# Performance work log

Hardware: AMD Instinct MI355X
Metric: run time of the kernel (lower is better)

The kernel has to match this reference:

```python
import jax, jax.numpy as jnp
import numpy as np
import math

NUM_HEADS = 16
D_MODEL = 1024
BATCH = 1
SEQ_LEN = 4096


def alibi_slopes(num_heads):
    # slopes m_h = (256 ** (1/H)) ** -(h+1)
    x = (2.0 ** 8) ** (1.0 / num_heads)
    return jnp.asarray([1.0 / x ** (i + 1) for i in range(num_heads)], dtype=jnp.float32)


def setup_inputs() -> dict:
    key = jax.random.key(0)
    k1, k2 = jax.random.split(key)
    x = jax.random.normal(k1, (BATCH, SEQ_LEN, D_MODEL), dtype=jnp.float32)
    # nn.Linear(d_model, 3*d_model, bias=False); store as [d_model, 3*d_model] so y = x @ w
    w_kqv = jax.random.normal(k2, (D_MODEL, 3 * D_MODEL), dtype=jnp.float32) * (1.0 / math.sqrt(D_MODEL))
    return {"x": x, "w_kqv": w_kqv}


def reference(x, w_kqv):
    B, S, D = x.shape
    H = NUM_HEADS
    dh = D // H
    scale = jnp.asarray(math.sqrt(D), dtype=x.dtype)  # module divides by sqrt(d_model)

    kqv = x @ w_kqv  # [B, S, 3D]
    # NOTE: original chunks as (key, query, value) in that order
    k, q, v = jnp.split(kqv, 3, axis=-1)
    q = q.reshape(B, S, H, dh)
    k = k.reshape(B, S, H, dh)
    v = v.reshape(B, S, H, dh)

    # ALiBi bias: m_h * (j - i), shape [H, S, S]
    pos = jnp.arange(S)
    rel = pos[None, :] - pos[:, None]  # [S, S], x - y
    slopes = alibi_slopes(H).astype(x.dtype)  # [H]
    bias = slopes[:, None, None] * rel.astype(x.dtype)  # [H, S, S]

    score = jnp.einsum('bihd,bjhd->bhij', q, k) / scale + bias[None]  # [B, H, S, S]
    causal = rel <= 0  # j <= i (lower triangular)
    score = jnp.where(causal[None, None], score, jnp.asarray(-jnp.inf, dtype=score.dtype))

    attn = jax.nn.softmax(score, axis=-1)
    out = jnp.einsum('bhij,bjhd->bihd', attn, v).reshape(B, S, D)
    return out
```

## Files before the change

kernel.cpp:

```cpp
#include <hip/hip_runtime.h>
#include <stdint.h>
#include <math.h>

#define SEQ 4096
#define DM  1024
#define NH  16
#define DH  64
#define LOG2E 1.44269504088896341f

typedef short bf16x8 __attribute__((ext_vector_type(8)));
typedef short bf16x4 __attribute__((ext_vector_type(4)));
typedef float f32x4  __attribute__((ext_vector_type(4)));
typedef uint32_t u32x4 __attribute__((ext_vector_type(4)));

typedef const __attribute__((address_space(1))) short* gptr_t;
typedef __attribute__((address_space(3))) short* lptr_t;

__device__ __forceinline__ short f2bf(float f) {
    union { float f; uint32_t u; } x; x.f = f;
    uint32_t r = (x.u + 0x7fffu + ((x.u >> 16) & 1u)) >> 16;
    return (short)r;
}
__device__ __forceinline__ uint32_t pkbf(float lo, float hi) {
    union { float f; uint32_t u; } a, b; a.f = lo; b.f = hi;
    return __builtin_amdgcn_perm(b.u, a.u, 0x07060302u);
}

__device__ __forceinline__ void load_lds16(const short* g, const short* l) {
    __builtin_amdgcn_global_load_lds((gptr_t)(uintptr_t)g,
                                     (lptr_t)(uint32_t)(uintptr_t)l, 16, 0, 0);
}

__device__ __forceinline__ void wgbar() {
    asm volatile("" ::: "memory");
    __builtin_amdgcn_s_barrier();
    asm volatile("" ::: "memory");
}
#define WAITVM(n) asm volatile("s_waitcnt vmcnt(" #n ")" ::: "memory")
#define WAITLGKM(n) do { asm volatile("s_waitcnt lgkmcnt(" #n ")" ::: "memory"); \
                         __builtin_amdgcn_sched_barrier(0); } while (0)
#define DSR(d, a, o) asm volatile("ds_read_b128 %0, %1 offset:" o : "=v"(d) : "v"(a))

__global__ __launch_bounds__(256) void cvt_fused(const float* __restrict__ x,
                                                 const float* __restrict__ w,
                                                 short* __restrict__ xb,
                                                 short* __restrict__ wtb) {
    __shared__ float T[64][69];
    const int b = blockIdx.x;
    if (b < 2048) {
        const int i = (b * 256 + threadIdx.x) * 8;
        float4 a0 = ((const float4*)(x + i))[0];
        float4 a1 = ((const float4*)(x + i))[1];
        bf16x8 p;
        p[0]=f2bf(a0.x); p[1]=f2bf(a0.y); p[2]=f2bf(a0.z); p[3]=f2bf(a0.w);
        p[4]=f2bf(a1.x); p[5]=f2bf(a1.y); p[6]=f2bf(a1.z); p[7]=f2bf(a1.w);
        *(bf16x8*)(xb + i) = p;
        return;
    }
    const int bb = b - 2048;
    const int n0 = (bb % 48) * 64, k0 = (bb / 48) * 64;
    const int t = threadIdx.x;
    {
        const int kr = t >> 4, nc = (t & 15) * 4;
        #pragma unroll
        for (int i = 0; i < 4; ++i) {
            float4 v = *(const float4*)(w + (size_t)(k0 + kr + i * 16) * 3072 + n0 + nc);
            T[kr + i * 16][nc + 0] = v.x; T[kr + i * 16][nc + 1] = v.y;
            T[kr + i * 16][nc + 2] = v.z; T[kr + i * 16][nc + 3] = v.w;
        }
    }
    __syncthreads();
    const int nr = t >> 4, kc = (t & 15) * 4;
    #pragma unroll
    for (int i = 0; i < 4; ++i) {
        const int n = n0 + nr + i * 16;
        const float sc = (n >= 1024 && n < 2048) ? (LOG2E / 32.0f) : 1.0f;
        short4 o;
        o.x = f2bf(T[kc + 0][nr + i * 16] * sc);
        o.y = f2bf(T[kc + 1][nr + i * 16] * sc);
        o.z = f2bf(T[kc + 2][nr + i * 16] * sc);
        o.w = f2bf(T[kc + 3][nr + i * 16] * sc);
        *(short4*)(wtb + (size_t)n * 1024 + k0 + kc) = o;
    }
}

__global__ __launch_bounds__(256, 2) void qkv_gemm(const short* __restrict__ xb,
                                                   const short* __restrict__ wtb,
                                                   short* __restrict__ kq,
                                                   short* __restrict__ vt) {
    __shared__ short As[2][8192];
    __shared__ short Bs[2][8192];
    const int col0 = blockIdx.y * 128, row0 = blockIdx.x * 128;
    const int tid = threadIdx.x, w = tid >> 6, lane = tid & 63;
    const int lmod = lane & 15, ldiv = lane >> 4;
    const int wr = (w >> 1) * 64, wc = (w & 1) * 64;

    const int srow = w * 32 + (lane >> 3);
    const int slc  = (lane & 7) ^ ((lane >> 3) & 7);
    const short* gA = xb  + (size_t)(row0 + srow) * 1024 + slc * 8;
    const short* gB = wtb + (size_t)(col0 + srow) * 1024 + slc * 8;
    short* lA = &As[0][0] + w * 2048;
    short* lB = &Bs[0][0] + w * 2048;

    const uint32_t asb = (uint32_t)(uintptr_t)&As[0][0];
    const uint32_t bsb = (uint32_t)(uintptr_t)&Bs[0][0];
    const int xorm = lmod & 7;
    const int rdA = (wr + lmod) * 128 + ((ldiv ^ xorm) << 4);
    const int rdB = (wc + lmod) * 128 + ((ldiv ^ xorm) << 4);

    f32x4 acc[4][4] = {};

    auto stage = [&](int kt, int p) {
        const short* ga = gA + kt * 64;
        const short* gb = gB + kt * 64;
        short* la = lA + p * 8192;
        short* lb = lB + p * 8192;
        #pragma unroll
        for (int q = 0; q < 4; ++q) {
            load_lds16(ga + q * 8192, la + q * 512);
            load_lds16(gb + q * 8192, lb + q * 512);
        }
    };

    stage(0, 0);
    stage(1, 1);
    WAITVM(8);
    wgbar();

    for (int t = 0; t < 16; ++t) {
        const int poff = (t & 1) << 14;
        const int aA0 = (int)asb + poff + rdA, aA1 = aA0 ^ 64;
        const int bA0 = (int)bsb + poff + rdB, bA1 = bA0 ^ 64;
        bf16x8 a0[4], a1[4], b0[4], b1[4];
        DSR(a0[0], aA0, "0");    DSR(a0[1], aA0, "2048");
        DSR(a0[2], aA0, "4096"); DSR(a0[3], aA0, "6144");
        DSR(b0[0], bA0, "0");    DSR(b0[1], bA0, "2048");
        DSR(b0[2], bA0, "4096"); DSR(b0[3], bA0, "6144");
        DSR(a1[0], aA1, "0");    DSR(a1[1], aA1, "2048");
        DSR(a1[2], aA1, "4096"); DSR(a1[3], aA1, "6144");
        DSR(b1[0], bA1, "0");    DSR(b1[1], bA1, "2048");
        DSR(b1[2], bA1, "4096"); DSR(b1[3], bA1, "6144");
        WAITLGKM(8);
        #pragma unroll
        for (int i = 0; i < 4; ++i)
            #pragma unroll
            for (int j = 0; j < 4; ++j)
                acc[i][j] = __builtin_amdgcn_mfma_f32_16x16x32_bf16(a0[i], b0[j], acc[i][j], 0, 0, 0);
        WAITLGKM(0);
        #pragma unroll
        for (int i = 0; i < 4; ++i)
            #pragma unroll
            for (int j = 0; j < 4; ++j)
                acc[i][j] = __builtin_amdgcn_mfma_f32_16x16x32_bf16(a1[i], b1[j], acc[i][j], 0, 0, 0);

        wgbar();
        if (t + 2 < 16) {
            stage(t + 2, t & 1);
            WAITVM(8);
            wgbar();
        } else if (t + 1 < 16) {
            WAITVM(0);
            wgbar();
        }
    }

    if (col0 < 2048) {
        #pragma unroll
        for (int i = 0; i < 4; ++i)
            #pragma unroll
            for (int j = 0; j < 4; ++j)
                #pragma unroll
                for (int r = 0; r < 4; ++r)
                    kq[(size_t)(row0 + wr + i * 16 + ldiv * 4 + r) * 2048
                       + col0 + wc + j * 16 + lmod] = f2bf(acc[i][j][r]);
    } else {
        #pragma unroll
        for (int i = 0; i < 4; ++i) {
            const int ig = row0 + wr + i * 16 + ldiv * 4;
            const int kk = ig & 63;
            const int kkp = (kk & 32) | ((kk & 12) << 1) | ((kk & 16) >> 2);
            const int igp = (ig & ~63) | kkp;
            #pragma unroll
            for (int j = 0; j < 4; ++j) {
                const int cg = col0 + wc + j * 16 + lmod - 2048;
                const int h = cg >> 6, d = cg & 63;
                bf16x4 p;
                p[0]=f2bf(acc[i][j][0]); p[1]=f2bf(acc[i][j][1]);
                p[2]=f2bf(acc[i][j][2]); p[3]=f2bf(acc[i][j][3]);
                *(bf16x4*)(vt + (size_t)(h * 64 + d) * SEQ + igp) = p;
            }
        }
    }
}

__global__ __launch_bounds__(256, 4) void attn(const short* __restrict__ kq,
                                               const short* __restrict__ vt,
                                               float* __restrict__ o0,
                                               float* __restrict__ o1,
                                               float* __restrict__ ls0,
                                               float* __restrict__ ls1) {
    __shared__ short Ks[64 * 64];
    __shared__ short Vs[64 * 64];

    const int b = blockIdx.x;
    const int band = b >> 8, pos = b & 255, g = pos >> 5;
    const int j = (band & 1) ? (56 - band * 8 + g) : (63 - band * 8 - g);
    const int h = (pos >> 1) & 15, s = pos & 1;

    const int tid = threadIdx.x, w = tid >> 6, lane = tid & 63;
    const int lmod = lane & 15, ldiv = lane >> 4;
    const float slope2 = exp2f(-0.5f * (float)(h + 1)) * LOG2E;

    const int sr0 = w * 16 + (lane >> 3), sr1 = sr0 + 8;
    const int sc0 = (lane & 7) ^ (sr0 & 7), sc1 = (lane & 7) ^ (sr1 & 7);

    const int xorm = lmod & 7;
    const int cxs0 = (ldiv ^ xorm) * 8;
    const int cxs1 = ((4 + ldiv) ^ xorm) * 8;

    const int rowbase = j * 64 + w * 16;

    bf16x8 qf[2];
    {
        const short* qp = kq + (size_t)(rowbase + lmod) * 2048 + 1024 + h * 64;
        qf[0] = *(const bf16x8*)(qp + ldiv * 8);
        qf[1] = *(const bf16x8*)(qp + 32 + ldiv * 8);
    }
    bf16x8 ones;
    #pragma unroll
    for (int e = 0; e < 8; ++e) ones[e] = (short)0x3F80;

    const int db2 = 4 * ldiv - (rowbase + lmod);
    float pre[4];
    #pragma unroll
    for (int r = 0; r < 4; ++r) pre[r] = slope2 * (float)(db2 + r);

    f32x4 O[4] = {};
    f32x4 lsacc = {};
    const int hh = (j + 2) >> 1;
    const int kt0 = s ? hh : 0;
    const int kt1 = s ? (j + 1) : hh;

    for (int kt = kt0; kt < kt1; ++kt) {
        __syncthreads();
        {
            const short* kb = kq + (size_t)(kt * 64) * 2048 + h * 64;
            load_lds16(kb + (size_t)sr0 * 2048 + sc0 * 8, Ks + (w * 16) * 64);
            load_lds16(kb + (size_t)sr1 * 2048 + sc1 * 8, Ks + (w * 16 + 8) * 64);
            const short* vb = vt + (size_t)(h * 64) * SEQ + kt * 64;
            load_lds16(vb + (size_t)sr0 * SEQ + sc0 * 8, Vs + (w * 16) * 64);
            load_lds16(vb + (size_t)sr1 * SEQ + sc1 * 8, Vs + (w * 16 + 8) * 64);
        }
        __syncthreads();

        const bool diag = (kt >= j);
        const int dt = kt * 64;
        const float cb = slope2 * (float)dt;

        #pragma unroll
        for (int ks = 0; ks < 2; ++ks) {
            u32x4 pk;
            #pragma unroll
            for (int j1 = 0; j1 < 2; ++j1) {
                const int nt = ks * 2 + j1;
                const float cn = cb + slope2 * (float)(nt * 16);
                f32x4 s0;
                #pragma unroll
                for (int r = 0; r < 4; ++r) s0[r] = pre[r] + cn;
                const short* krow = Ks + (nt * 16 + lmod) * 64;
                const bf16x8 kf0 = *(const bf16x8*)(krow + cxs0);
                const bf16x8 kf1 = *(const bf16x8*)(krow + cxs1);
                s0 = __builtin_amdgcn_mfma_f32_16x16x32_bf16(kf0, qf[0], s0, 0, 0, 0);
                s0 = __builtin_amdgcn_mfma_f32_16x16x32_bf16(kf1, qf[1], s0, 0, 0, 0);

                float p0[4];
                if (diag) {
                    #pragma unroll
                    for (int r = 0; r < 4; ++r) {
                        float v0 = s0[r];
                        if (dt + nt * 16 + r + db2 > 0) v0 = -1e30f;
                        p0[r] = __builtin_amdgcn_exp2f(v0);
                    }
                } else {
                    #pragma unroll
                    for (int r = 0; r < 4; ++r)
                        p0[r] = __builtin_amdgcn_exp2f(s0[r]);
                }
                pk[j1 * 2]     = pkbf(p0[0], p0[1]);
                pk[j1 * 2 + 1] = pkbf(p0[2], p0[3]);
            }
            const bf16x8 pa = __builtin_bit_cast(bf16x8, pk);
            const int cxo = ks ? cxs1 : cxs0;
            lsacc = __builtin_amdgcn_mfma_f32_16x16x32_bf16(pa, ones, lsacc, 0, 0, 0);
            #pragma unroll
            for (int nt2 = 0; nt2 < 4; ++nt2) {
                const bf16x8 vf = *(const bf16x8*)(Vs + (nt2 * 16 + lmod) * 64 + cxo);
                O[nt2] = __builtin_amdgcn_mfma_f32_16x16x32_bf16(pa, vf, O[nt2], 0, 0, 0);
            }
        }
    }

    float* ob = s ? o1 : o0;
    float* lb = s ? ls1 : ls0;
    const int i0 = rowbase + ldiv * 4;
    #pragma unroll
    for (int nt2 = 0; nt2 < 4; ++nt2)
        #pragma unroll
        for (int r = 0; r < 4; ++r)
            ob[(size_t)(i0 + r) * DM + h * 64 + nt2 * 16 + lmod] = O[nt2][r];
    if (lmod == 0) {
        #pragma unroll
        for (int r = 0; r < 4; ++r)
            lb[h * SEQ + i0 + r] = lsacc[r];
    }
}

__global__ __launch_bounds__(256) void combine(float* __restrict__ out,
                                               const float* __restrict__ opart,
                                               const float* __restrict__ ls0,
                                               const float* __restrict__ ls1) {
    const int i8 = (blockIdx.x * 256 + threadIdx.x) * 8;
    const int row = i8 >> 10, col = i8 & 1023, h = col >> 6;
    const float l = ls0[h * SEQ + row] + ls1[h * SEQ + row];
    const float rc = 1.0f / l;
    float4 a0 = *(const float4*)(out + i8);
    float4 a1 = *(const float4*)(out + i8 + 4);
    float4 b0 = *(const float4*)(opart + i8);
    float4 b1 = *(const float4*)(opart + i8 + 4);
    float4 c0, c1;
    c0.x = (a0.x + b0.x) * rc; c0.y = (a0.y + b0.y) * rc;
    c0.z = (a0.z + b0.z) * rc; c0.w = (a0.w + b0.w) * rc;
    c1.x = (a1.x + b1.x) * rc; c1.y = (a1.y + b1.y) * rc;
    c1.z = (a1.z + b1.z) * rc; c1.w = (a1.w + b1.w) * rc;
    *(float4*)(out + i8) = c0;
    *(float4*)(out + i8 + 4) = c1;
}

extern "C" void kernel_launch(void* const* d_in, const int* in_sizes, int n_in,
                              void* d_out, int out_size, void* d_ws, size_t ws_size,
                              hipStream_t stream) {
    const float* x = (const float*)d_in[0];
    const float* w = (const float*)d_in[1];
    float* out = (float*)d_out;

    char* ws = (char*)d_ws;
    short* kq    = (short*)(ws);
    short* vt    = (short*)(ws + ((size_t)16 << 20));
    short* xb    = (short*)(ws + ((size_t)24 << 20));
    short* wtb   = (short*)(ws + ((size_t)32 << 20));
    float* opart = (float*)(ws + ((size_t)24 << 20));
    float* ls0   = (float*)(ws + ((size_t)40 << 20));
    float* ls1   = (float*)(ws + ((size_t)40 << 20) + (256 << 10));

    cvt_fused<<<2048 + 768, 256, 0, stream>>>(x, w, xb, wtb);
    qkv_gemm <<<dim3(SEQ / 128, 3072 / 128), 256, 0, stream>>>(xb, wtb, kq, vt);
    attn     <<<2048, 256, 0, stream>>>(kq, vt, out, opart, ls0, ls1);
    combine  <<<SEQ * DM / (256 * 8), 256, 0, stream>>>(out, opart, ls0, ls1);
}
```

Before: 160.9 us.

## Drop split-K attention and combine kernel; normalize in attention epilogue

Removes the two-way split of each query tile's key range, so each block now processes the full causal key range, and the launch goes from 2048 to 1024 blocks. The separate combine kernel and its partial-output and row-sum buffers are gone: each block divides by its row sum and writes the final output directly. A new band-to-tile mapping pairs long and short query tiles for load balance. This removes a kernel launch and the partial-result memory traffic, but halves the number of blocks, so per-block work is longer and more uneven across the machine.

```diff
diff --git a/kernel.cpp b/kernel.cpp
--- a/kernel.cpp
+++ b/kernel.cpp
@@ -195,17 +195,24 @@
 
 __global__ __launch_bounds__(256, 4) void attn(const short* __restrict__ kq,
                                                const short* __restrict__ vt,
-                                               float* __restrict__ o0,
-                                               float* __restrict__ o1,
-                                               float* __restrict__ ls0,
-                                               float* __restrict__ ls1) {
+                                               float* __restrict__ out) {
     __shared__ short Ks[64 * 64];
     __shared__ short Vs[64 * 64];
 
     const int b = blockIdx.x;
-    const int band = b >> 8, pos = b & 255, g = pos >> 5;
-    const int j = (band & 1) ? (56 - band * 8 + g) : (63 - band * 8 - g);
-    const int h = (pos >> 1) & 15, s = pos & 1;
+    const int band = b >> 7, pos = b & 127;
+    const int g = pos >> 4, h = pos & 15;
+    int j;
+    switch (band) {
+        case 0:  j = 63 - g; break;
+        case 1:  j = 55 - g; break;
+        case 2:  j = 40 + g; break;
+        case 3:  j = 32 + g; break;
+        case 4:  j = 23 - g; break;
+        case 5:  j = 31 - g; break;
+        case 6:  j = g;      break;
+        default: j = 8 + g;  break;
+    }
 
     const int tid = threadIdx.x, w = tid >> 6, lane = tid & 63;
     const int lmod = lane & 15, ldiv = lane >> 4;
@@ -237,11 +244,8 @@
 
     f32x4 O[4] = {};
     f32x4 lsacc = {};
-    const int hh = (j + 2) >> 1;
-    const int kt0 = s ? hh : 0;
-    const int kt1 = s ? (j + 1) : hh;
-
-    for (int kt = kt0; kt < kt1; ++kt) {
+
+    for (int kt = 0; kt <= j; ++kt) {
         __syncthreads();
         {
             const short* kb = kq + (size_t)(kt * 64) * 2048 + h * 64;
@@ -300,40 +304,16 @@
         }
     }
 
-    float* ob = s ? o1 : o0;
-    float* lb = s ? ls1 : ls0;
+    float rc[4];
+    #pragma unroll
+    for (int r = 0; r < 4; ++r) rc[r] = 1.0f / lsacc[r];
+
     const int i0 = rowbase + ldiv * 4;
     #pragma unroll
     for (int nt2 = 0; nt2 < 4; ++nt2)
         #pragma unroll
         for (int r = 0; r < 4; ++r)
-            ob[(size_t)(i0 + r) * DM + h * 64 + nt2 * 16 + lmod] = O[nt2][r];
-    if (lmod == 0) {
-        #pragma unroll
-        for (int r = 0; r < 4; ++r)
-            lb[h * SEQ + i0 + r] = lsacc[r];
-    }
-}
-
-__global__ __launch_bounds__(256) void combine(float* __restrict__ out,
-                                               const float* __restrict__ opart,
-                                               const float* __restrict__ ls0,
-                                               const float* __restrict__ ls1) {
-    const int i8 = (blockIdx.x * 256 + threadIdx.x) * 8;
-    const int row = i8 >> 10, col = i8 & 1023, h = col >> 6;
-    const float l = ls0[h * SEQ + row] + ls1[h * SEQ + row];
-    const float rc = 1.0f / l;
-    float4 a0 = *(const float4*)(out + i8);
-    float4 a1 = *(const float4*)(out + i8 + 4);
-    float4 b0 = *(const float4*)(opart + i8);
-    float4 b1 = *(const float4*)(opart + i8 + 4);
-    float4 c0, c1;
-    c0.x = (a0.x + b0.x) * rc; c0.y = (a0.y + b0.y) * rc;
-    c0.z = (a0.z + b0.z) * rc; c0.w = (a0.w + b0.w) * rc;
-    c1.x = (a1.x + b1.x) * rc; c1.y = (a1.y + b1.y) * rc;
-    c1.z = (a1.z + b1.z) * rc; c1.w = (a1.w + b1.w) * rc;
-    *(float4*)(out + i8) = c0;
-    *(float4*)(out + i8 + 4) = c1;
+            out[(size_t)(i0 + r) * DM + h * 64 + nt2 * 16 + lmod] = O[nt2][r] * rc[r];
 }
 
 extern "C" void kernel_launch(void* const* d_in, const int* in_sizes, int n_in,
@@ -348,12 +328,8 @@
     short* vt    = (short*)(ws + ((size_t)16 << 20));
     short* xb    = (short*)(ws + ((size_t)24 << 20));
     short* wtb   = (short*)(ws + ((size_t)32 << 20));
-    float* opart = (float*)(ws + ((size_t)24 << 20));
-    float* ls0   = (float*)(ws + ((size_t)40 << 20));
-    float* ls1   = (float*)(ws + ((size_t)40 << 20) + (256 << 10));
 
     cvt_fused<<<2048 + 768, 256, 0, stream>>>(x, w, xb, wtb);
     qkv_gemm <<<dim3(SEQ / 128, 3072 / 128), 256, 0, stream>>>(xb, wtb, kq, vt);
-    attn     <<<2048, 256, 0, stream>>>(kq, vt, out, opart, ls0, ls1);
-    combine  <<<SEQ * DM / (256 * 8), 256, 0, stream>>>(out, opart, ls0, ls1);
-}
+    attn     <<<1024, 256, 0, stream>>>(kq, vt, out);
+}
```

Result: no change. 163.4 us (+1.5%).
